# Performance work log

Hardware: AMD Instinct MI355X
Metric: run time of the kernel (lower is better)

## Reference

```python
import jax, jax.numpy as jnp
import numpy as np

B, NC, A = 16, 80, 33600          # batch, num_classes, num_anchors
CLS_CH, REG_CH = 256, 256
TOPK_PRE, TOPK_POST = 750, 30
IOU_THRESH = 0.4                   # nms_thresh_val (module in eval mode)


def setup_inputs() -> dict:
    key = jax.random.key(0)
    k1, k2, k3, k4, k5 = jax.random.split(key, 5)
    # Build raw_preds so the first 4 channels are valid x1,y1,x2,y2 boxes
    xy = jax.random.uniform(k1, (B, 2, A)) * 600.0
    wh = jax.random.uniform(k2, (B, 2, A)) * 40.0 + 1.0
    boxes = jnp.concatenate([xy, xy + wh], axis=1)            # [B,4,A]
    cls_scores = jax.random.uniform(k3, (B, NC, A))            # sigmoid-like in [0,1)
    raw_preds = jnp.concatenate([boxes, cls_scores], axis=1).astype(jnp.float32)
    vid_features = jax.random.normal(k4, (B, A, CLS_CH), jnp.float32)
    reg_features = jax.random.normal(k5, (B, A, REG_CH), jnp.float32)
    return {"raw_preds": raw_preds, "vid_features": vid_features, "reg_features": reg_features}


def _nms_keep(boxes, cls_ids, iou_thresh):
    """torchvision.batched_nms: offset boxes per class so cross-class IoU == 0.
    boxes: [N,4] x1y1x2y2 sorted by descending score. Returns keep mask [N]."""
    max_coord = boxes.max()
    off = cls_ids.astype(boxes.dtype) * (max_coord + 1.0)
    b = boxes + off[:, None]
    x1, y1, x2, y2 = b[:, 0], b[:, 1], b[:, 2], b[:, 3]
    area = (x2 - x1) * (y2 - y1)
    iw = jnp.clip(jnp.minimum(x2[:, None], x2[None, :]) - jnp.maximum(x1[:, None], x1[None, :]), 0.0)
    ih = jnp.clip(jnp.minimum(y2[:, None], y2[None, :]) - jnp.maximum(y1[:, None], y1[None, :]), 0.0)
    inter = iw * ih
    iou = inter / (area[:, None] + area[None, :] - inter)     # [N,N]
    N = boxes.shape[0]
    idxs = jnp.arange(N)

    def body(i, keep):
        sup = keep[i] & (iou[i] > iou_thresh) & (idxs > i)
        return keep & jnp.logical_not(sup)

    return jax.lax.fori_loop(0, N, body, jnp.ones((N,), bool))


def _select_frame(boxes_b, max_scores_b, cls_ids_b):
    # top-k pre-NMS (sorted by descending score, like torch.topk)
    _, topk_idx = jax.lax.top_k(max_scores_b, TOPK_PRE)
    bsel = boxes_b[topk_idx]
    csel = cls_ids_b[topk_idx]
    keep = _nms_keep(bsel, csel, IOU_THRESH)
    # kept indices in score order; take first TOPK_POST (stable argsort: kept first)
    order = jnp.argsort(jnp.logical_not(keep))[:TOPK_POST]
    return topk_idx[order]                                    # [TOPK_POST]


def reference(raw_preds, vid_features, reg_features):
    preds = jnp.transpose(raw_preds, (0, 2, 1))               # [B,A,4+NC]
    boxes = preds[..., :4]
    scores = preds[..., 4:]
    max_scores = scores.max(axis=-1)                          # [B,A]
    cls_ids = jnp.argmax(scores, axis=-1)                     # [B,A]
    final_idx = jax.vmap(_select_frame)(boxes, max_scores, cls_ids)   # [B,TOPK_POST]

    gat = lambda f: jnp.take_along_axis(f, final_idx[..., None], axis=1)
    cls_f = gat(vid_features).reshape(1, -1, CLS_CH)          # [1,B*30,256]
    reg_f = gat(reg_features).reshape(1, -1, REG_CH)          # [1,B*30,256]
    box_f = gat(boxes).reshape(1, -1, 4)                      # [1,B*30,4]
    sc_f = jnp.take_along_axis(max_scores, final_idx, axis=1).reshape(1, -1)  # [1,B*30]
    return cls_f, reg_f, box_f, sc_f
```

## Files before the change

### kernel.cpp

```cpp
#include <hip/hip_runtime.h>
#include <stdint.h>

#pragma clang fp contract(off)

#define BB 16
#define NCC 80
#define AA 33600
#define TOPK_PRE 750
#define TOPK_POST 30
#define NBINS 16384
#define CAND 1024
#define NW 12

__global__ __launch_bounds__(256) void k_scoremax(const float* __restrict__ raw,
                                                  float* __restrict__ maxs,
                                                  int* __restrict__ clsid,
                                                  unsigned int* __restrict__ hist) {
  int gid = blockIdx.x * blockDim.x + threadIdx.x;
  if (gid >= BB * AA) return;
  int b = gid / AA, a = gid - b * AA;
  const float* p = raw + (size_t)b * 84 * AA + (size_t)4 * AA + a;
  float best = -1e30f; int bc = 0;
  for (int c = 0; c < NCC; ++c) {
    float s = p[(size_t)c * AA];
    if (s > best) { best = s; bc = c; }
  }
  maxs[gid] = best;
  clsid[gid] = bc;
  int d = 0x3F800000 - (int)__float_as_uint(best);
  if (d < 0) d = 0;
  if (d < NBINS - 1) atomicAdd(&hist[b * NBINS + d], 1u);
}

__global__ __launch_bounds__(256) void k_select(const float* __restrict__ maxs,
                                                const int* __restrict__ clsid,
                                                const unsigned int* __restrict__ hist,
                                                const float* __restrict__ raw,
                                                int* __restrict__ topk,
                                                float* __restrict__ sx1, float* __restrict__ sy1,
                                                float* __restrict__ sx2, float* __restrict__ sy2,
                                                float* __restrict__ sarea) {
  int b = blockIdx.x;
  int tid = threadIdx.x;
  __shared__ unsigned int psum[256];
  __shared__ unsigned int pref[256];
  __shared__ int s_cut;
  __shared__ unsigned int s_cnt;
  __shared__ unsigned int keys[CAND];
  __shared__ float red[256];

  const unsigned int* h = hist + b * NBINS;
  unsigned int part = 0;
  for (int i = 0; i < 64; ++i) part += h[tid * 64 + i];
  psum[tid] = part;
  if (tid == 0) { s_cut = NBINS - 1; s_cnt = 0; }
  __syncthreads();
  if (tid == 0) {
    unsigned int run = 0;
    for (int t = 0; t < 256; ++t) { pref[t] = run; run += psum[t]; }
  }
  __syncthreads();
  unsigned int base = pref[tid];
  if (base < TOPK_PRE && base + part >= TOPK_PRE) {
    unsigned int run = base;
    for (int i = 0; i < 64; ++i) {
      run += h[tid * 64 + i];
      if (run >= TOPK_PRE) { s_cut = tid * 64 + i; break; }
    }
  }
  for (int i = tid; i < CAND; i += 256) keys[i] = 0xFFFFFFFFu;
  __syncthreads();

  int cut = s_cut;
  for (int a = tid; a < AA; a += 256) {
    float v = maxs[(size_t)b * AA + a];
    int d = 0x3F800000 - (int)__float_as_uint(v);
    if (d >= 0 && d <= cut) {
      unsigned int pos = atomicAdd(&s_cnt, 1u);
      if (pos < CAND) keys[pos] = ((unsigned int)d << 16) | (unsigned int)a;
    }
  }
  __syncthreads();

  for (int k = 2; k <= CAND; k <<= 1) {
    for (int j = k >> 1; j > 0; j >>= 1) {
      for (int s = tid; s < CAND; s += 256) {
        int p = s ^ j;
        if (p > s) {
          unsigned int x = keys[s], y = keys[p];
          bool up = ((s & k) == 0);
          if ((x > y) == up) { keys[s] = y; keys[p] = x; }
        }
      }
      __syncthreads();
    }
  }

  float lx1[3], ly1[3], lx2[3], ly2[3];
  int lcl[3];
  float m = -1e30f;
#pragma unroll
  for (int r = 0; r < 3; ++r) {
    int i = tid + r * 256;
    if (i < TOPK_PRE) {
      int a = (int)(keys[i] & 0xFFFFu);
      topk[b * TOPK_PRE + i] = a;
      const float* p = raw + (size_t)b * 84 * AA + a;
      float x1 = p[0], y1 = p[AA], x2 = p[2 * AA], y2 = p[3 * AA];
      lx1[r] = x1; ly1[r] = y1; lx2[r] = x2; ly2[r] = y2;
      lcl[r] = clsid[(size_t)b * AA + a];
      m = fmaxf(m, fmaxf(fmaxf(x1, y1), fmaxf(x2, y2)));
    }
  }
  red[tid] = m;
  __syncthreads();
  for (int s = 128; s > 0; s >>= 1) {
    if (tid < s) red[tid] = fmaxf(red[tid], red[tid + s]);
    __syncthreads();
  }
  float mc1 = red[0] + 1.0f;
#pragma unroll
  for (int r = 0; r < 3; ++r) {
    int i = tid + r * 256;
    if (i < TOPK_PRE) {
      float off = (float)lcl[r] * mc1;
      float X1 = lx1[r] + off, Y1 = ly1[r] + off, X2 = lx2[r] + off, Y2 = ly2[r] + off;
      int o = b * TOPK_PRE + i;
      sx1[o] = X1; sy1[o] = Y1; sx2[o] = X2; sy2[o] = Y2;
      sarea[o] = (X2 - X1) * (Y2 - Y1);
    }
  }
}

__global__ __launch_bounds__(256) void k_iou(const float* __restrict__ sx1, const float* __restrict__ sy1,
                                             const float* __restrict__ sx2, const float* __restrict__ sy2,
                                             const float* __restrict__ sarea,
                                             unsigned long long* __restrict__ mask) {
  int i = blockIdx.x, b = blockIdx.y;
  int base = b * TOPK_PRE;
  float x1i = sx1[base + i], y1i = sy1[base + i];
  float x2i = sx2[base + i], y2i = sy2[base + i];
  float ai = sarea[base + i];
  int tid = threadIdx.x;
#pragma unroll
  for (int it = 0; it < 3; ++it) {
    int j = it * 256 + tid;
    bool sup = false;
    if (j > i && j < TOPK_PRE) {
      float iw = fminf(x2i, sx2[base + j]) - fmaxf(x1i, sx1[base + j]);
      iw = fmaxf(iw, 0.0f);
      float ih = fminf(y2i, sy2[base + j]) - fmaxf(y1i, sy1[base + j]);
      ih = fmaxf(ih, 0.0f);
      float inter = iw * ih;
      float denom = (ai + sarea[base + j]) - inter;
      sup = (inter / denom) > 0.4f;
    }
    unsigned long long bal = __ballot(sup);
    if ((tid & 63) == 0)
      mask[((size_t)(b * TOPK_PRE + i)) * NW + it * 4 + (tid >> 6)] = bal;
  }
}

__global__ __launch_bounds__(64) void k_nmsreduce(const unsigned long long* __restrict__ mask,
                                                  const int* __restrict__ topk,
                                                  int* __restrict__ finalidx) {
  int b = blockIdx.x;
  int lane = threadIdx.x;
  unsigned long long kw = ~0ULL;
  const unsigned long long* m = mask + (size_t)b * TOPK_PRE * NW;
  for (int i = 0; i < TOPK_PRE; ++i) {
    unsigned long long cur = __shfl(kw, i >> 6);
    if ((cur >> (i & 63)) & 1ULL) {
      if (lane < NW) kw &= ~m[(size_t)i * NW + lane];
    }
  }
  int cnt = 0;
  for (int i = 0; i < TOPK_PRE && cnt < TOPK_POST; ++i) {
    unsigned long long cur = __shfl(kw, i >> 6);
    if ((cur >> (i & 63)) & 1ULL) {
      if (lane == 0) finalidx[b * TOPK_POST + cnt] = topk[b * TOPK_PRE + i];
      cnt++;
    }
  }
  for (int i = 0; i < TOPK_PRE && cnt < TOPK_POST; ++i) {
    unsigned long long cur = __shfl(kw, i >> 6);
    if (!((cur >> (i & 63)) & 1ULL)) {
      if (lane == 0) finalidx[b * TOPK_POST + cnt] = topk[b * TOPK_PRE + i];
      cnt++;
    }
  }
}

__global__ __launch_bounds__(256) void k_gather(const float* __restrict__ vid,
                                                const float* __restrict__ reg,
                                                const float* __restrict__ raw,
                                                const float* __restrict__ maxs,
                                                const int* __restrict__ finalidx,
                                                float* __restrict__ out) {
  int r = blockIdx.x;
  int b = r / TOPK_POST;
  int a = finalidx[r];
  int t = threadIdx.x;
  size_t src = ((size_t)b * AA + a) * 256 + t;
  out[(size_t)r * 256 + t] = vid[src];
  out[122880 + (size_t)r * 256 + t] = reg[src];
  if (t < 4) out[245760 + r * 4 + t] = raw[(size_t)b * 84 * AA + (size_t)t * AA + a];
  if (t == 4) out[247680 + r] = maxs[(size_t)b * AA + a];
}

extern "C" void kernel_launch(void* const* d_in, const int* in_sizes, int n_in,
                              void* d_out, int out_size, void* d_ws, size_t ws_size,
                              hipStream_t stream) {
  const float* raw = (const float*)d_in[0];
  const float* vid = (const float*)d_in[1];
  const float* reg = (const float*)d_in[2];
  float* out = (float*)d_out;

  char* ws = (char*)d_ws;
  size_t off = 0;
  auto alloc = [&](size_t nbytes) -> void* {
    void* p = ws + off;
    off = (off + nbytes + 255) & ~(size_t)255;
    return p;
  };
  float* maxs = (float*)alloc((size_t)BB * AA * 4);
  int* clsid = (int*)alloc((size_t)BB * AA * 4);
  unsigned int* hist = (unsigned int*)alloc((size_t)BB * NBINS * 4);
  int* topk = (int*)alloc((size_t)BB * TOPK_PRE * 4);
  float* sx1 = (float*)alloc((size_t)BB * TOPK_PRE * 4);
  float* sy1 = (float*)alloc((size_t)BB * TOPK_PRE * 4);
  float* sx2 = (float*)alloc((size_t)BB * TOPK_PRE * 4);
  float* sy2 = (float*)alloc((size_t)BB * TOPK_PRE * 4);
  float* sarea = (float*)alloc((size_t)BB * TOPK_PRE * 4);
  unsigned long long* mask = (unsigned long long*)alloc((size_t)BB * TOPK_PRE * NW * 8);
  int* finalidx = (int*)alloc((size_t)BB * TOPK_POST * 4);

  hipMemsetAsync(hist, 0, (size_t)BB * NBINS * 4, stream);

  int total = BB * AA;
  k_scoremax<<<(total + 255) / 256, 256, 0, stream>>>(raw, maxs, clsid, hist);
  k_select<<<BB, 256, 0, stream>>>(maxs, clsid, hist, raw, topk, sx1, sy1, sx2, sy2, sarea);
  k_iou<<<dim3(TOPK_PRE, BB), 256, 0, stream>>>(sx1, sy1, sx2, sy2, sarea, mask);
  k_nmsreduce<<<BB, 64, 0, stream>>>(mask, topk, finalidx);
  k_gather<<<BB * TOPK_POST, 256, 0, stream>>>(vid, reg, raw, maxs, finalidx, out);
}
```

Measured before the change: 1.173 ms.

## Fuse top-k select and NMS into one kernel with early exit; vectorize score max

Merges the select, pairwise-IoU and NMS-reduce kernels into one block-per-frame kernel. Candidate boxes stay in shared memory, and greedy suppression runs directly and stops once the post-NMS quota of kept boxes is reached. This removes the full IoU bitmask pass, its global traffic and a serial reduce loop that walked every candidate. Separately, the score-max kernel now handles four anchors per thread with float4 loads. In exchange, NMS runs sequentially inside one block per frame, and the shared `s_cnt` read/increment pattern across iterations is fragile.

```diff
diff --git a/kernel.cpp b/kernel.cpp
--- a/kernel.cpp
+++ b/kernel.cpp
@@ -6,54 +6,65 @@
 #define BB 16
 #define NCC 80
 #define AA 33600
+#define A4 (AA / 4)
 #define TOPK_PRE 750
 #define TOPK_POST 30
 #define NBINS 16384
 #define CAND 1024
-#define NW 12
 
 __global__ __launch_bounds__(256) void k_scoremax(const float* __restrict__ raw,
                                                   float* __restrict__ maxs,
                                                   int* __restrict__ clsid,
                                                   unsigned int* __restrict__ hist) {
   int gid = blockIdx.x * blockDim.x + threadIdx.x;
-  if (gid >= BB * AA) return;
-  int b = gid / AA, a = gid - b * AA;
-  const float* p = raw + (size_t)b * 84 * AA + (size_t)4 * AA + a;
-  float best = -1e30f; int bc = 0;
+  if (gid >= BB * A4) return;
+  int b = gid / A4, a4 = (gid - b * A4) * 4;
+  const float* p = raw + (size_t)b * 84 * AA + (size_t)4 * AA + a4;
+  float4 best = make_float4(-1e30f, -1e30f, -1e30f, -1e30f);
+  int bc0 = 0, bc1 = 0, bc2 = 0, bc3 = 0;
   for (int c = 0; c < NCC; ++c) {
-    float s = p[(size_t)c * AA];
-    if (s > best) { best = s; bc = c; }
-  }
-  maxs[gid] = best;
-  clsid[gid] = bc;
-  int d = 0x3F800000 - (int)__float_as_uint(best);
-  if (d < 0) d = 0;
-  if (d < NBINS - 1) atomicAdd(&hist[b * NBINS + d], 1u);
-}
-
-__global__ __launch_bounds__(256) void k_select(const float* __restrict__ maxs,
-                                                const int* __restrict__ clsid,
-                                                const unsigned int* __restrict__ hist,
-                                                const float* __restrict__ raw,
-                                                int* __restrict__ topk,
-                                                float* __restrict__ sx1, float* __restrict__ sy1,
-                                                float* __restrict__ sx2, float* __restrict__ sy2,
-                                                float* __restrict__ sarea) {
+    float4 s = *(const float4*)(p + (size_t)c * AA);
+    if (s.x > best.x) { best.x = s.x; bc0 = c; }
+    if (s.y > best.y) { best.y = s.y; bc1 = c; }
+    if (s.z > best.z) { best.z = s.z; bc2 = c; }
+    if (s.w > best.w) { best.w = s.w; bc3 = c; }
+  }
+  *(float4*)(maxs + (size_t)b * AA + a4) = best;
+  *(int4*)(clsid + (size_t)b * AA + a4) = make_int4(bc0, bc1, bc2, bc3);
+  unsigned int* h = hist + b * NBINS;
+  int d0 = 0x3F800000 - (int)__float_as_uint(best.x);
+  int d1 = 0x3F800000 - (int)__float_as_uint(best.y);
+  int d2 = 0x3F800000 - (int)__float_as_uint(best.z);
+  int d3 = 0x3F800000 - (int)__float_as_uint(best.w);
+  if (d0 >= 0 && d0 < NBINS - 1) atomicAdd(&h[d0], 1u);
+  if (d1 >= 0 && d1 < NBINS - 1) atomicAdd(&h[d1], 1u);
+  if (d2 >= 0 && d2 < NBINS - 1) atomicAdd(&h[d2], 1u);
+  if (d3 >= 0 && d3 < NBINS - 1) atomicAdd(&h[d3], 1u);
+}
+
+__global__ __launch_bounds__(256) void k_selectnms(const float* __restrict__ maxs,
+                                                   const int* __restrict__ clsid,
+                                                   const unsigned int* __restrict__ hist,
+                                                   const float* __restrict__ raw,
+                                                   int* __restrict__ finalidx) {
   int b = blockIdx.x;
   int tid = threadIdx.x;
   __shared__ unsigned int psum[256];
   __shared__ unsigned int pref[256];
   __shared__ int s_cut;
-  __shared__ unsigned int s_cnt;
+  __shared__ unsigned int s_cnt0;
   __shared__ unsigned int keys[CAND];
   __shared__ float red[256];
+  __shared__ float bx1[TOPK_PRE], by1[TOPK_PRE], bx2[TOPK_PRE], by2[TOPK_PRE], barea[TOPK_PRE];
+  __shared__ int s_keep[TOPK_PRE];
+  __shared__ int s_out[TOPK_POST];
+  __shared__ int s_cnt;
 
   const unsigned int* h = hist + b * NBINS;
   unsigned int part = 0;
   for (int i = 0; i < 64; ++i) part += h[tid * 64 + i];
   psum[tid] = part;
-  if (tid == 0) { s_cut = NBINS - 1; s_cnt = 0; }
+  if (tid == 0) { s_cut = NBINS - 1; s_cnt0 = 0; s_cnt = 0; }
   __syncthreads();
   if (tid == 0) {
     unsigned int run = 0;
@@ -76,7 +87,7 @@
     float v = maxs[(size_t)b * AA + a];
     int d = 0x3F800000 - (int)__float_as_uint(v);
     if (d >= 0 && d <= cut) {
-      unsigned int pos = atomicAdd(&s_cnt, 1u);
+      unsigned int pos = atomicAdd(&s_cnt0, 1u);
       if (pos < CAND) keys[pos] = ((unsigned int)d << 16) | (unsigned int)a;
     }
   }
@@ -104,7 +115,6 @@
     int i = tid + r * 256;
     if (i < TOPK_PRE) {
       int a = (int)(keys[i] & 0xFFFFu);
-      topk[b * TOPK_PRE + i] = a;
       const float* p = raw + (size_t)b * 84 * AA + a;
       float x1 = p[0], y1 = p[AA], x2 = p[2 * AA], y2 = p[3 * AA];
       lx1[r] = x1; ly1[r] = y1; lx2[r] = x2; ly2[r] = y2;
@@ -125,70 +135,36 @@
     if (i < TOPK_PRE) {
       float off = (float)lcl[r] * mc1;
       float X1 = lx1[r] + off, Y1 = ly1[r] + off, X2 = lx2[r] + off, Y2 = ly2[r] + off;
-      int o = b * TOPK_PRE + i;
-      sx1[o] = X1; sy1[o] = Y1; sx2[o] = X2; sy2[o] = Y2;
-      sarea[o] = (X2 - X1) * (Y2 - Y1);
-    }
-  }
-}
-
-__global__ __launch_bounds__(256) void k_iou(const float* __restrict__ sx1, const float* __restrict__ sy1,
-                                             const float* __restrict__ sx2, const float* __restrict__ sy2,
-                                             const float* __restrict__ sarea,
-                                             unsigned long long* __restrict__ mask) {
-  int i = blockIdx.x, b = blockIdx.y;
-  int base = b * TOPK_PRE;
-  float x1i = sx1[base + i], y1i = sy1[base + i];
-  float x2i = sx2[base + i], y2i = sy2[base + i];
-  float ai = sarea[base + i];
-  int tid = threadIdx.x;
-#pragma unroll
-  for (int it = 0; it < 3; ++it) {
-    int j = it * 256 + tid;
-    bool sup = false;
-    if (j > i && j < TOPK_PRE) {
-      float iw = fminf(x2i, sx2[base + j]) - fmaxf(x1i, sx1[base + j]);
-      iw = fmaxf(iw, 0.0f);
-      float ih = fminf(y2i, sy2[base + j]) - fmaxf(y1i, sy1[base + j]);
-      ih = fmaxf(ih, 0.0f);
-      float inter = iw * ih;
-      float denom = (ai + sarea[base + j]) - inter;
-      sup = (inter / denom) > 0.4f;
-    }
-    unsigned long long bal = __ballot(sup);
-    if ((tid & 63) == 0)
-      mask[((size_t)(b * TOPK_PRE + i)) * NW + it * 4 + (tid >> 6)] = bal;
-  }
-}
-
-__global__ __launch_bounds__(64) void k_nmsreduce(const unsigned long long* __restrict__ mask,
-                                                  const int* __restrict__ topk,
-                                                  int* __restrict__ finalidx) {
-  int b = blockIdx.x;
-  int lane = threadIdx.x;
-  unsigned long long kw = ~0ULL;
-  const unsigned long long* m = mask + (size_t)b * TOPK_PRE * NW;
+      bx1[i] = X1; by1[i] = Y1; bx2[i] = X2; by2[i] = Y2;
+      barea[i] = (X2 - X1) * (Y2 - Y1);
+    }
+  }
+  for (int i = tid; i < TOPK_PRE; i += 256) s_keep[i] = 1;
+  __syncthreads();
+
   for (int i = 0; i < TOPK_PRE; ++i) {
-    unsigned long long cur = __shfl(kw, i >> 6);
-    if ((cur >> (i & 63)) & 1ULL) {
-      if (lane < NW) kw &= ~m[(size_t)i * NW + lane];
-    }
-  }
-  int cnt = 0;
-  for (int i = 0; i < TOPK_PRE && cnt < TOPK_POST; ++i) {
-    unsigned long long cur = __shfl(kw, i >> 6);
-    if ((cur >> (i & 63)) & 1ULL) {
-      if (lane == 0) finalidx[b * TOPK_POST + cnt] = topk[b * TOPK_PRE + i];
-      cnt++;
-    }
-  }
-  for (int i = 0; i < TOPK_PRE && cnt < TOPK_POST; ++i) {
-    unsigned long long cur = __shfl(kw, i >> 6);
-    if (!((cur >> (i & 63)) & 1ULL)) {
-      if (lane == 0) finalidx[b * TOPK_POST + cnt] = topk[b * TOPK_PRE + i];
-      cnt++;
-    }
-  }
+    if (s_keep[i]) {
+      float X1 = bx1[i], Y1 = by1[i], X2 = bx2[i], Y2 = by2[i], Ai = barea[i];
+      for (int j = i + 1 + tid; j < TOPK_PRE; j += 256) {
+        float iw = fmaxf(fminf(X2, bx2[j]) - fmaxf(X1, bx1[j]), 0.0f);
+        float ih = fmaxf(fminf(Y2, by2[j]) - fmaxf(Y1, by1[j]), 0.0f);
+        float inter = iw * ih;
+        float denom = (Ai + barea[j]) - inter;
+        if (inter / denom > 0.4f) s_keep[j] = 0;
+      }
+      if (tid == 0) s_out[s_cnt++] = i;
+      __syncthreads();
+      if (s_cnt >= TOPK_POST) break;
+    }
+  }
+
+  if (tid == 0) {
+    int c = s_cnt;
+    for (int j = 0; j < TOPK_PRE && c < TOPK_POST; ++j)
+      if (!s_keep[j]) s_out[c++] = j;
+  }
+  __syncthreads();
+  if (tid < TOPK_POST) finalidx[b * TOPK_POST + tid] = (int)(keys[s_out[tid]] & 0xFFFFu);
 }
 
 __global__ __launch_bounds__(256) void k_gather(const float* __restrict__ vid,
@@ -226,21 +202,11 @@
   float* maxs = (float*)alloc((size_t)BB * AA * 4);
   int* clsid = (int*)alloc((size_t)BB * AA * 4);
   unsigned int* hist = (unsigned int*)alloc((size_t)BB * NBINS * 4);
-  int* topk = (int*)alloc((size_t)BB * TOPK_PRE * 4);
-  float* sx1 = (float*)alloc((size_t)BB * TOPK_PRE * 4);
-  float* sy1 = (float*)alloc((size_t)BB * TOPK_PRE * 4);
-  float* sx2 = (float*)alloc((size_t)BB * TOPK_PRE * 4);
-  float* sy2 = (float*)alloc((size_t)BB * TOPK_PRE * 4);
-  float* sarea = (float*)alloc((size_t)BB * TOPK_PRE * 4);
-  unsigned long long* mask = (unsigned long long*)alloc((size_t)BB * TOPK_PRE * NW * 8);
   int* finalidx = (int*)alloc((size_t)BB * TOPK_POST * 4);
 
   hipMemsetAsync(hist, 0, (size_t)BB * NBINS * 4, stream);
 
-  int total = BB * AA;
-  k_scoremax<<<(total + 255) / 256, 256, 0, stream>>>(raw, maxs, clsid, hist);
-  k_select<<<BB, 256, 0, stream>>>(maxs, clsid, hist, raw, topk, sx1, sy1, sx2, sy2, sarea);
-  k_iou<<<dim3(TOPK_PRE, BB), 256, 0, stream>>>(sx1, sy1, sx2, sy2, sarea, mask);
-  k_nmsreduce<<<BB, 64, 0, stream>>>(mask, topk, finalidx);
+  k_scoremax<<<(BB * A4 + 255) / 256, 256, 0, stream>>>(raw, maxs, clsid, hist);
+  k_selectnms<<<BB, 256, 0, stream>>>(maxs, clsid, hist, raw, finalidx);
   k_gather<<<BB * TOPK_POST, 256, 0, stream>>>(vid, reg, raw, maxs, finalidx, out);
 }
```

After: 1.008 ms. 14.0% less time.
